# Performance work log

Hardware: AMD Instinct MI355X
Metric: run time of the kernel (lower is better)

The kernel has to match this reference:

```python
import jax, jax.numpy as jnp
import numpy as np

B, H, W, C = 4, 64, 64, 1280
NH = 16          # num heads
HD = C // NH     # 80 features per head
WS = 14          # window size
REL = 2 * WS - 1 # 27 relative-position entries per axis
EPS = 1e-6


def setup_inputs() -> dict:
    key = jax.random.key(0)
    ks = jax.random.split(key, 16)
    s = 0.02
    return {
        "imagelike_bhwc": jax.random.normal(ks[0], (B, H, W, C), jnp.float32),
        "ln1_g": jnp.ones((C,), jnp.float32),
        "ln1_b": jnp.zeros((C,), jnp.float32),
        "qkv_w": jax.random.normal(ks[1], (C, 3 * C), jnp.float32) * s,
        "qkv_b": jnp.zeros((3 * C,), jnp.float32),
        "proj_w": jax.random.normal(ks[2], (C, C), jnp.float32) * s,
        "proj_b": jnp.zeros((C,), jnp.float32),
        "rel_pos_h": jax.random.normal(ks[3], (REL, HD), jnp.float32) * s,
        "rel_pos_w": jax.random.normal(ks[4], (REL, HD), jnp.float32) * s,
        "ln2_g": jnp.ones((C,), jnp.float32),
        "ln2_b": jnp.zeros((C,), jnp.float32),
        "mlp_w1": jax.random.normal(ks[5], (C, 4 * C), jnp.float32) * s,
        "mlp_b1": jnp.zeros((4 * C,), jnp.float32),
        "mlp_w2": jax.random.normal(ks[6], (4 * C, C), jnp.float32) * s,
        "mlp_b2": jnp.zeros((C,), jnp.float32),
    }


def _layernorm(t, g, b):
    mu = jnp.mean(t, axis=-1, keepdims=True)
    var = jnp.var(t, axis=-1, keepdims=True)
    return (t - mu) * jax.lax.rsqrt(var + EPS) * g + b


def reference(imagelike_bhwc, ln1_g, ln1_b, qkv_w, qkv_b, proj_w, proj_b,
              rel_pos_h, rel_pos_w, ln2_g, ln2_b, mlp_w1, mlp_b1, mlp_w2, mlp_b2):
    x = imagelike_bhwc
    b, h, w, c = x.shape
    hd = c // NH
    scale = hd ** -0.5
    # --- image -> windows (pad to multiple of WS) ---
    hp, wp = (-h) % WS, (-w) % WS
    xp = jnp.pad(x, ((0, 0), (0, hp), (0, wp), (0, 0)))
    Hp, Wp = h + hp, w + wp
    ny, nx = Hp // WS, Wp // WS
    win = xp.reshape(b, ny, WS, nx, WS, c).transpose(0, 1, 3, 2, 4, 5)
    win = win.reshape(b * ny * nx, WS, WS, c)      # (Bw, S, S, C)
    Bw, N = win.shape[0], WS * WS
    # --- pre-attention layernorm + qkv ---
    t = _layernorm(win, ln1_g, ln1_b)
    qkv = t.reshape(Bw, N, c) @ qkv_w + qkv_b      # (Bw, N, 3C)
    qkv = qkv.reshape(Bw, N, 3, NH, hd).transpose(2, 0, 3, 1, 4)  # (3,Bw,NH,N,hd)
    q, k, v = qkv[0], qkv[1], qkv[2]
    # --- scores + decomposed relative position bias ---
    attn = jnp.einsum('bhqd,bhkd->bhqk', q * scale, k)            # (Bw,NH,N,N)
    idx = jnp.arange(WS)[:, None] - jnp.arange(WS)[None, :] + (WS - 1)
    Rh = rel_pos_h[idx]                                           # (WS,WS,hd)
    Rw = rel_pos_w[idx]                                           # (WS,WS,hd)
    qr = q.reshape(Bw, NH, WS, WS, hd)
    bias_h = jnp.einsum('bnyxd,ykd->bnyxk', qr, Rh)               # (Bw,NH,WS,WS,WS)
    bias_w = jnp.einsum('bnyxd,xkd->bnyxk', qr, Rw)
    bias = (bias_h[..., :, None] + bias_w[..., None, :]).reshape(Bw, NH, N, N)
    attn = jax.nn.softmax(attn + bias, axis=-1)
    out = jnp.einsum('bhqk,bhkd->bhqd', attn, v)                  # (Bw,NH,N,hd)
    out = out.transpose(0, 2, 1, 3).reshape(Bw, WS, WS, c)
    out = out @ proj_w + proj_b
    attn_out = out + win                                          # residual 1
    # --- MLP ---
    t2 = _layernorm(attn_out, ln2_g, ln2_b)
    mlp = jax.nn.gelu(t2 @ mlp_w1 + mlp_b1, approximate=False) @ mlp_w2 + mlp_b2
    out = mlp + attn_out                                          # residual 2
    # --- windows -> image (remove padding) ---
    img = out.reshape(b, ny, nx, WS, WS, c).transpose(0, 1, 3, 2, 4, 5)
    img = img.reshape(b, Hp, Wp, c)
    return img[:, :h, :w, :]
```

## Files before the change

kernel.cpp:

```cpp
#include <hip/hip_runtime.h>

typedef __attribute__((ext_vector_type(8))) short short8;
typedef __attribute__((ext_vector_type(4))) float f32x4;

#define GLBP(p) ((const __attribute__((address_space(1))) void*)(p))
#define LDSP(p) ((__attribute__((address_space(3))) void*)(p))

__device__ __forceinline__ float bf2f(unsigned short u) {
  return __uint_as_float(((unsigned int)u) << 16);
}
__device__ __forceinline__ unsigned short f2bf(float f) {
  unsigned int u = __float_as_uint(f);
  u += 0x7fff + ((u >> 16) & 1);
  return (unsigned short)(u >> 16);
}

__device__ __forceinline__ void tok2pix(int gt, int& b, int& py, int& px) {
  int w = gt / 196, t = gt - w * 196;
  b = w / 25;
  int wr = w - b * 25;
  int wy = wr / 5, wx = wr - wy * 5;
  int ty = t / 14;
  py = wy * 14 + ty;
  px = wx * 14 + (t - ty * 14);
}

__global__ void k_transpose(const float* __restrict__ W, unsigned short* __restrict__ Wt,
                            int K, int N) {
  __shared__ float tile[32][33];
  int tx = threadIdx.x, ty = threadIdx.y;
  int n0 = blockIdx.x * 32, k0 = blockIdx.y * 32;
#pragma unroll
  for (int i = 0; i < 4; ++i)
    tile[ty + 8 * i][tx] = W[(size_t)(k0 + ty + 8 * i) * N + n0 + tx];
  __syncthreads();
#pragma unroll
  for (int i = 0; i < 4; ++i)
    Wt[(size_t)(n0 + ty + 8 * i) * K + k0 + tx] = f2bf(tile[tx][ty + 8 * i]);
}

__global__ __launch_bounds__(256) void k_ln1(const float* __restrict__ x,
                                             const float* __restrict__ g,
                                             const float* __restrict__ be,
                                             unsigned short* __restrict__ A1,
                                             int w0, int ctok) {
  int m = blockIdx.x * 4 + (threadIdx.x >> 6);
  int lane = threadIdx.x & 63;
  int b, py, px;
  tok2pix(w0 * 196 + m, b, py, px);
  bool valid = (m < ctok) && (py < 64) && (px < 64);
  const float* row = x + ((size_t)((b * 64 + py) * 64 + px)) * 1280;
  float v[20];
#pragma unroll
  for (int i = 0; i < 20; ++i) v[i] = valid ? row[lane + 64 * i] : 0.f;
  float s = 0.f, ss = 0.f;
#pragma unroll
  for (int i = 0; i < 20; ++i) { s += v[i]; ss += v[i] * v[i]; }
#pragma unroll
  for (int o = 32; o > 0; o >>= 1) { s += __shfl_down(s, o); ss += __shfl_down(ss, o); }
  s = __shfl(s, 0);
  ss = __shfl(ss, 0);
  float mu = s * (1.f / 1280.f);
  float var = ss * (1.f / 1280.f) - mu * mu;
  float rinv = rsqrtf(var + 1e-6f);
  unsigned short* o1 = A1 + (size_t)m * 1280;
#pragma unroll
  for (int i = 0; i < 20; ++i) {
    int c = lane + 64 * i;
    o1[c] = f2bf((v[i] - mu) * rinv * g[c] + be[c]);
  }
}

__global__ __launch_bounds__(256) void k_ln2(const float* __restrict__ AT,
                                             const float* __restrict__ g,
                                             const float* __restrict__ be,
                                             unsigned short* __restrict__ A2,
                                             int w0, int ctok) {
  int m = blockIdx.x * 4 + (threadIdx.x >> 6);
  int lane = threadIdx.x & 63;
  int b, py, px;
  tok2pix(w0 * 196 + m, b, py, px);
  bool valid = (m < ctok) && (py < 64) && (px < 64);
  const float* row = AT + ((size_t)((b * 64 + py) * 64 + px)) * 1280;
  float v[20];
#pragma unroll
  for (int i = 0; i < 20; ++i) v[i] = valid ? row[lane + 64 * i] : 0.f;
  float s = 0.f, ss = 0.f;
#pragma unroll
  for (int i = 0; i < 20; ++i) { s += v[i]; ss += v[i] * v[i]; }
#pragma unroll
  for (int o = 32; o > 0; o >>= 1) { s += __shfl_down(s, o); ss += __shfl_down(ss, o); }
  s = __shfl(s, 0);
  ss = __shfl(ss, 0);
  float mu = s * (1.f / 1280.f);
  float var = ss * (1.f / 1280.f) - mu * mu;
  float rinv = rsqrtf(var + 1e-6f);
  unsigned short* o1 = A2 + (size_t)m * 1280;
#pragma unroll
  for (int i = 0; i < 20; ++i) {
    int c = lane + 64 * i;
    o1[c] = f2bf((v[i] - mu) * rinv * g[c] + be[c]);
  }
}

template <int EPI>
__device__ __forceinline__ void gemm_body(const unsigned short* __restrict__ A,
                                          const unsigned short* __restrict__ Bt,
                                          int K, int N, int gx,
                                          const float* __restrict__ bias,
                                          void* __restrict__ outp, int ctok) {
  __shared__ __align__(16) char smem[73728];
  int tid = threadIdx.x;
  int w = tid >> 6, lane = tid & 63;
  int nwg = gridDim.x, bid = blockIdx.x;
  int q = nwg >> 3, r = nwg & 7;
  int xcd = bid & 7, loc = bid >> 3;
  int wg = (xcd < r ? xcd * (q + 1) : r * (q + 1) + (xcd - r) * q) + loc;
  int bx = wg % gx, by = wg / gx;
  int mBase = by * 256, nBase = bx * 128;
  int wr = w >> 2, wc = w & 3;
  int la = lane & 15, lg = lane >> 4;

  int srow = tid >> 2;
  int schunk = (tid & 3) ^ ((srow >> 1) & 3);
  const char* pa0 = (const char*)A + (size_t)(mBase + srow) * K * 2 + (schunk << 4);
  const char* pa1 = (const char*)A + (size_t)(mBase + 128 + srow) * K * 2 + (schunk << 4);
  const char* pb0 = (const char*)Bt + (size_t)(nBase + srow) * K * 2 + (schunk << 4);
  int ldst = tid * 16;

  auto STAGE = [&](int slot, size_t ko) {
    int b = slot * 24576;
    __builtin_amdgcn_global_load_lds(GLBP(pa0 + ko), LDSP(smem + b + ldst), 16, 0, 0);
    __builtin_amdgcn_global_load_lds(GLBP(pa1 + ko), LDSP(smem + b + 8192 + ldst), 16, 0, 0);
    __builtin_amdgcn_global_load_lds(GLBP(pb0 + ko), LDSP(smem + b + 16384 + ldst), 16, 0, 0);
  };

  int offA[8], offB[2];
#pragma unroll
  for (int m = 0; m < 8; ++m) {
    int rr = wr * 128 + m * 16 + la;
    offA[m] = rr * 64 + ((lg ^ ((rr >> 1) & 3)) << 4);
  }
#pragma unroll
  for (int n = 0; n < 2; ++n) {
    int rr = wc * 32 + n * 16 + la;
    offB[n] = 16384 + rr * 64 + ((lg ^ ((rr >> 1) & 3)) << 4);
  }

  const f32x4 z4 = {0.f, 0.f, 0.f, 0.f};
  f32x4 acc[8][2];
#pragma unroll
  for (int m = 0; m < 8; ++m)
#pragma unroll
    for (int n = 0; n < 2; ++n) acc[m][n] = z4;

  int NT = K >> 5;
  STAGE(0, 0);
  STAGE(1, 64);
  int rs = 0;
  for (int t = 0; t < NT; ++t) {
    if (t + 1 < NT)
      asm volatile("s_waitcnt vmcnt(3)" ::: "memory");
    else
      asm volatile("s_waitcnt vmcnt(0)" ::: "memory");
    __builtin_amdgcn_s_barrier();
    __builtin_amdgcn_sched_barrier(0);
    if (t + 2 < NT) {
      int ws = rs + 2;
      if (ws >= 3) ws -= 3;
      STAGE(ws, (size_t)(t + 2) * 64);
    }
    const char* buf = (const char*)smem + rs * 24576;
    short8 af[4], bfr[2];
#pragma unroll
    for (int n = 0; n < 2; ++n) bfr[n] = *(const short8*)(buf + offB[n]);
#pragma unroll
    for (int m = 0; m < 4; ++m) af[m] = *(const short8*)(buf + offA[m]);
    __builtin_amdgcn_s_setprio(1);
#pragma unroll
    for (int m = 0; m < 4; ++m)
#pragma unroll
      for (int n = 0; n < 2; ++n)
        acc[m][n] = __builtin_amdgcn_mfma_f32_16x16x32_bf16(af[m], bfr[n], acc[m][n], 0, 0, 0);
    __builtin_amdgcn_s_setprio(0);
    __builtin_amdgcn_sched_barrier(0);
#pragma unroll
    for (int m = 0; m < 4; ++m) af[m] = *(const short8*)(buf + offA[m + 4]);
    __builtin_amdgcn_s_setprio(1);
#pragma unroll
    for (int m = 0; m < 4; ++m)
#pragma unroll
      for (int n = 0; n < 2; ++n)
        acc[m + 4][n] = __builtin_amdgcn_mfma_f32_16x16x32_bf16(af[m], bfr[n], acc[m + 4][n], 0, 0, 0);
    __builtin_amdgcn_s_setprio(0);
    rs = (rs == 2) ? 0 : rs + 1;
  }

#pragma unroll
  for (int m = 0; m < 8; ++m) {
#pragma unroll
    for (int n = 0; n < 2; ++n) {
      int col = nBase + wc * 32 + n * 16 + la;
      float bcol = bias[col];
#pragma unroll
      for (int j = 0; j < 4; ++j) {
        int row = mBase + wr * 128 + m * 16 + lg * 4 + j;
        float v = acc[m][n][j] + bcol;
        if (EPI == 0) {
          if (row < ctok) {
            int wloc = row / 196, tt = row - wloc * 196;
            int which = col / 1280, cr = col - which * 1280;
            int nh = cr / 80, d = cr - nh * 80;
            ((unsigned short*)outp)[((((size_t)wloc * 16 + nh) * 3 + which) * 196 + tt) * 80 + d] =
                f2bf(v);
          }
        } else {
          float gg = 0.5f * v * (1.f + erff(v * 0.70710678118654752f));
          ((unsigned short*)outp)[(size_t)row * N + col] = f2bf(gg);
        }
      }
    }
  }
}

template <int EPI>
__device__ __forceinline__ void gemm128_body(const unsigned short* __restrict__ A,
                                             const unsigned short* __restrict__ Bt,
                                             int K, int N, int gx,
                                             const float* __restrict__ bias,
                                             float* __restrict__ outp,
                                             const float* __restrict__ xres,
                                             int w0, int ctok) {
  __shared__ __align__(16) char smem[49152];
  int tid = threadIdx.x;
  int w = tid >> 6, lane = tid & 63;
  int nwg = gridDim.x, bid = blockIdx.x;
  int q = nwg >> 3, r = nwg & 7;
  int xcd = bid & 7, loc = bid >> 3;
  int wg = (xcd < r ? xcd * (q + 1) : r * (q + 1) + (xcd - r) * q) + loc;
  int bx = wg % gx, by = wg / gx;
  int mBase = by * 128, nBase = bx * 128;
  int wr = w >> 1, wc = w & 1;
  int la = lane & 15, lg = lane >> 4;

  int srow = tid >> 2;
  int schunk = (tid & 3) ^ ((srow >> 1) & 3);
  const char* pa[2];
  const char* pb[2];
#pragma unroll
  for (int i = 0; i < 2; ++i) {
    pa[i] = (const char*)A + (size_t)(mBase + srow + i * 64) * K * 2 + (schunk << 4);
    pb[i] = (const char*)Bt + (size_t)(nBase + srow + i * 64) * K * 2 + (schunk << 4);
  }
  int ldst = tid * 16;

  auto STAGE = [&](int slot, size_t ko) {
    int b = slot * 16384;
#pragma unroll
    for (int i = 0; i < 2; ++i)
      __builtin_amdgcn_global_load_lds(GLBP(pa[i] + ko), LDSP(smem + b + i * 4096 + ldst), 16, 0, 0);
#pragma unroll
    for (int i = 0; i < 2; ++i)
      __builtin_amdgcn_global_load_lds(GLBP(pb[i] + ko), LDSP(smem + b + 8192 + i * 4096 + ldst), 16, 0, 0);
  };

  int offA[4], offB[4];
#pragma unroll
  for (int m = 0; m < 4; ++m) {
    int rr = wr * 64 + m * 16 + la;
    offA[m] = rr * 64 + ((lg ^ ((rr >> 1) & 3)) << 4);
  }
#pragma unroll
  for (int n = 0; n < 4; ++n) {
    int rr = wc * 64 + n * 16 + la;
    offB[n] = 8192 + rr * 64 + ((lg ^ ((rr >> 1) & 3)) << 4);
  }

  const f32x4 z4 = {0.f, 0.f, 0.f, 0.f};
  f32x4 acc[4][4];
#pragma unroll
  for (int m = 0; m < 4; ++m)
#pragma unroll
    for (int n = 0; n < 4; ++n) acc[m][n] = z4;

  int NT = K >> 5;
  STAGE(0, 0);
  STAGE(1, 64);
  int rs = 0;
  for (int t = 0; t < NT; ++t) {
    if (t + 1 < NT)
      asm volatile("s_waitcnt vmcnt(4)" ::: "memory");
    else
      asm volatile("s_waitcnt vmcnt(0)" ::: "memory");
    __builtin_amdgcn_s_barrier();
    __builtin_amdgcn_sched_barrier(0);
    if (t + 2 < NT) {
      int ws = rs + 2;
      if (ws >= 3) ws -= 3;
      STAGE(ws, (size_t)(t + 2) * 64);
    }
    const char* buf = (const char*)smem + rs * 16384;
    short8 af[4], bfr[4];
#pragma unroll
    for (int n = 0; n < 4; ++n) bfr[n] = *(const short8*)(buf + offB[n]);
#pragma unroll
    for (int m = 0; m < 4; ++m) af[m] = *(const short8*)(buf + offA[m]);
    __builtin_amdgcn_s_setprio(1);
#pragma unroll
    for (int m = 0; m < 4; ++m)
#pragma unroll
      for (int n = 0; n < 4; ++n)
        acc[m][n] = __builtin_amdgcn_mfma_f32_16x16x32_bf16(af[m], bfr[n], acc[m][n], 0, 0, 0);
    __builtin_amdgcn_s_setprio(0);
    rs = (rs == 2) ? 0 : rs + 1;
  }

#pragma unroll
  for (int m = 0; m < 4; ++m) {
#pragma unroll
    for (int n = 0; n < 4; ++n) {
      int col = nBase + wc * 64 + n * 16 + la;
      float bcol = bias[col];
#pragma unroll
      for (int j = 0; j < 4; ++j) {
        int row = mBase + wr * 64 + m * 16 + lg * 4 + j;
        if (row < ctok) {
          int b, py, px;
          tok2pix(w0 * 196 + row, b, py, px);
          if (py < 64 && px < 64) {
            size_t pix = ((size_t)((b * 64 + py) * 64 + px)) * 1280 + col;
            float v = acc[m][n][j] + bcol;
            if (EPI == 1)
              outp[pix] = v + xres[pix];
            else
              outp[pix] = v + outp[pix];
          }
        }
      }
    }
  }
}

__global__ __launch_bounds__(512, 4) void k_gqkv(const unsigned short* A, const unsigned short* Bt,
                                                 int K, int N, int gx, const float* bias, void* o,
                                                 int ct) {
  gemm_body<0>(A, Bt, K, N, gx, bias, o, ct);
}
__global__ __launch_bounds__(512, 4) void k_gmlp1(const unsigned short* A, const unsigned short* Bt,
                                                  int K, int N, int gx, const float* bias, void* o,
                                                  int ct) {
  gemm_body<2>(A, Bt, K, N, gx, bias, o, ct);
}
__global__ __launch_bounds__(256, 3) void k_gproj(const unsigned short* A, const unsigned short* Bt,
                                                  int K, int N, int gx, const float* bias, float* o,
                                                  const float* xr, int w0, int ct) {
  gemm128_body<1>(A, Bt, K, N, gx, bias, o, xr, w0, ct);
}
__global__ __launch_bounds__(256, 3) void k_gmlp2(const unsigned short* A, const unsigned short* Bt,
                                                  int K, int N, int gx, const float* bias, float* o,
                                                  const float* xr, int w0, int ct) {
  gemm128_body<3>(A, Bt, K, N, gx, bias, o, xr, w0, ct);
}

__global__ __launch_bounds__(512, 1) void k_attn(const unsigned short* __restrict__ qkv,
                                                 const float* __restrict__ rph,
                                                 const float* __restrict__ rpw,
                                                 unsigned short* __restrict__ AO) {
  __shared__ unsigned short Ks[208 * 104];
  __shared__ unsigned short Vt[80 * 232];
  __shared__ unsigned short Ps[8][16 * 232];
  __shared__ unsigned short Bls[196 * 28];
  int wh = blockIdx.x;
  int w = wh >> 4, nh = wh & 15;
  int tid = threadIdx.x, wid = tid >> 6, lane = tid & 63;
  int la = lane & 15, lg = lane >> 4;
  const unsigned short* qb = qkv + (size_t)wh * 47040;
  const unsigned short* kb = qb + 15680;
  const unsigned short* vb = qb + 31360;
  const short8 z8 = {0, 0, 0, 0, 0, 0, 0, 0};

  for (int c = tid; c < 208 * 13; c += 512) {
    int t = c / 13, seg = c - t * 13;
    short8 kv = z8;
    if (t < 196 && seg < 10) kv = *(const short8*)(kb + (size_t)t * 80 + seg * 8);
    *(short8*)(Ks + t * 104 + seg * 8) = kv;
  }
  for (int c = tid; c < 1960; c += 512) {
    int t = c / 10, d8 = (c - t * 10) * 8;
    short8 vv = *(const short8*)(vb + (size_t)t * 80 + d8);
#pragma unroll
    for (int e = 0; e < 8; ++e) Vt[(d8 + e) * 232 + t] = (unsigned short)vv[e];
  }
  for (int i = tid; i < 80 * 36; i += 512) Vt[(i / 36) * 232 + 196 + (i % 36)] = 0;
  for (int id = tid; id < 196 * 28; id += 512) {
    int t = id / 28, c = id - t * 28;
    int y = t / 14, xx = t - y * 14;
    const float* R = (c < 14) ? (rph + (size_t)(y - c + 13) * 80)
                              : (rpw + (size_t)(xx - (c - 14) + 13) * 80);
    const unsigned short* qq = qb + (size_t)t * 80;
    float acc = 0.f;
#pragma unroll
    for (int d8 = 0; d8 < 10; ++d8) {
      short8 qv = *(const short8*)(qq + d8 * 8);
      const float4* Rv = (const float4*)(R + d8 * 8);
      float4 ra = Rv[0], rb = Rv[1];
      acc += bf2f((unsigned short)qv[0]) * ra.x + bf2f((unsigned short)qv[1]) * ra.y +
             bf2f((unsigned short)qv[2]) * ra.z + bf2f((unsigned short)qv[3]) * ra.w +
             bf2f((unsigned short)qv[4]) * rb.x + bf2f((unsigned short)qv[5]) * rb.y +
             bf2f((unsigned short)qv[6]) * rb.z + bf2f((unsigned short)qv[7]) * rb.w;
    }
    Bls[id] = f2bf(acc);
  }
  __syncthreads();

  int kyv[13], kxv[13];
#pragma unroll
  for (int ci = 0; ci < 13; ++ci) {
    int key = ci * 16 + la;
    kyv[ci] = key / 14;
    kxv[ci] = key - kyv[ci] * 14;
  }

  const float scale = 0.111803398874989485f;
  const f32x4 z4 = {0.f, 0.f, 0.f, 0.f};
  unsigned short* P = Ps[wid];

  auto process = [&](int rb) {
    short8 qa[3];
    int tq = rb * 16 + la;
    if (tq >= 196) tq = 0;
#pragma unroll
    for (int kk = 0; kk < 3; ++kk) {
      int d = kk * 32 + lg * 8;
      qa[kk] = (kk < 2 || lg < 2) ? *(const short8*)(qb + (size_t)tq * 80 + d) : z8;
    }
    f32x4 s[13];
#pragma unroll
    for (int i = 0; i < 13; ++i) s[i] = z4;
#pragma unroll
    for (int kk = 0; kk < 3; ++kk) {
#pragma unroll
      for (int ni = 0; ni < 13; ++ni) {
        short8 bb = *(const short8*)(Ks + (ni * 16 + la) * 104 + kk * 32 + lg * 8);
        s[ni] = __builtin_amdgcn_mfma_f32_16x16x32_bf16(qa[kk], bb, s[ni], 0, 0, 0);
      }
    }
#pragma unroll
    for (int j = 0; j < 4; ++j) {
      int rloc = lg * 4 + j;
      int t = rb * 16 + rloc;
      bool tval = t < 196;
      const unsigned short* Bp = Bls + (tval ? t : 0) * 28;
      float v[13];
      float mx = -3e30f;
#pragma unroll
      for (int ci = 0; ci < 13; ++ci) {
        int key = ci * 16 + la;
        float val = s[ci][j] * scale;
        if (key < 196 && tval) val += bf2f(Bp[kyv[ci]]) + bf2f(Bp[14 + kxv[ci]]);
        if (key >= 196 || !tval) val = -3e30f;
        v[ci] = val;
        mx = fmaxf(mx, val);
      }
#pragma unroll
      for (int o = 1; o < 16; o <<= 1) mx = fmaxf(mx, __shfl_xor(mx, o));
      float sum = 0.f;
#pragma unroll
      for (int ci = 0; ci < 13; ++ci) {
        float e = __expf(v[ci] - mx);
        v[ci] = e;
        sum += e;
      }
#pragma unroll
      for (int o = 1; o < 16; o <<= 1) sum += __shfl_xor(sum, o);
      float inv = 1.f / sum;
#pragma unroll
      for (int ci = 0; ci < 13; ++ci) P[rloc * 232 + ci * 16 + la] = f2bf(v[ci] * inv);
      P[rloc * 232 + 208 + la] = 0;
    }
    f32x4 o5[5];
#pragma unroll
    for (int i = 0; i < 5; ++i) o5[i] = z4;
#pragma unroll
    for (int kc = 0; kc < 7; ++kc) {
      short8 aa = *(const short8*)(P + la * 232 + kc * 32 + lg * 8);
#pragma unroll
      for (int ni = 0; ni < 5; ++ni) {
        short8 bb = *(const short8*)(Vt + (ni * 16 + la) * 232 + kc * 32 + lg * 8);
        o5[ni] = __builtin_amdgcn_mfma_f32_16x16x32_bf16(aa, bb, o5[ni], 0, 0, 0);
      }
    }
#pragma unroll
    for (int ni = 0; ni < 5; ++ni)
#pragma unroll
      for (int j = 0; j < 4; ++j) {
        int t = rb * 16 + lg * 4 + j;
        if (t < 196)
          AO[((size_t)w * 196 + t) * 1280 + nh * 80 + ni * 16 + la] = f2bf(o5[ni][j]);
      }
  };

  process(wid);
  if (wid < 5) process(wid + 8);
}

extern "C" void kernel_launch(void* const* d_in, const int* in_sizes, int n_in,
                              void* d_out, int out_size, void* d_ws, size_t ws_size,
                              hipStream_t stream) {
  const float* x = (const float*)d_in[0];
  const float* ln1g = (const float*)d_in[1];
  const float* ln1b = (const float*)d_in[2];
  const float* qkvw = (const float*)d_in[3];
  const float* qkvb = (const float*)d_in[4];
  const float* projw = (const float*)d_in[5];
  const float* projb = (const float*)d_in[6];
  const float* rph = (const float*)d_in[7];
  const float* rpw = (const float*)d_in[8];
  const float* ln2g = (const float*)d_in[9];
  const float* ln2b = (const float*)d_in[10];
  const float* w1 = (const float*)d_in[11];
  const float* b1 = (const float*)d_in[12];
  const float* w2 = (const float*)d_in[13];
  const float* b2 = (const float*)d_in[14];
  float* out = (float*)d_out;

  const size_t woff = (3840ull * 1280 + 1280ull * 1280 + 5120ull * 1280 + 1280ull * 5120) * 2;
  const int NWopts[12] = {25, 20, 18, 16, 14, 12, 10, 8, 5, 4, 2, 1};
  int NW = 0, Mb = 0;
  for (int i = 0; i < 12; ++i) {
    int nw = NWopts[i];
    int mb = ((nw * 196 + 255) / 256) * 256;
    size_t tot = woff + (size_t)mb * 12800;
    if (tot <= ws_size) { NW = nw; Mb = mb; break; }
  }
  if (!NW) return;

  char* p = (char*)d_ws;
  unsigned short* qkvwT = (unsigned short*)p; p += 3840ull * 1280 * 2;
  unsigned short* projwT = (unsigned short*)p; p += 1280ull * 1280 * 2;
  unsigned short* w1T = (unsigned short*)p; p += 5120ull * 1280 * 2;
  unsigned short* w2T = (unsigned short*)p; p += 1280ull * 5120 * 2;
  unsigned short* A1 = (unsigned short*)p; p += (size_t)Mb * 2560;
  unsigned short* QKV = (unsigned short*)p; p += (size_t)Mb * 7680;
  unsigned short* AO = (unsigned short*)p;
  unsigned short* Hb = QKV;
  unsigned short* A2 = A1;

  k_transpose<<<dim3(120, 40), dim3(32, 8), 0, stream>>>(qkvw, qkvwT, 1280, 3840);
  k_transpose<<<dim3(40, 40), dim3(32, 8), 0, stream>>>(projw, projwT, 1280, 1280);
  k_transpose<<<dim3(160, 40), dim3(32, 8), 0, stream>>>(w1, w1T, 1280, 5120);
  k_transpose<<<dim3(40, 160), dim3(32, 8), 0, stream>>>(w2, w2T, 5120, 1280);

  int gy256 = Mb / 256, gy128 = Mb / 128;
  int nchunks = (100 + NW - 1) / NW;
  for (int c = 0; c < nchunks; ++c) {
    int w0 = c * NW;
    int cw = (100 - w0 < NW) ? (100 - w0) : NW;
    int ctok = cw * 196;
    k_ln1<<<Mb / 4, 256, 0, stream>>>(x, ln1g, ln1b, A1, w0, ctok);
    k_gqkv<<<30 * gy256, 512, 0, stream>>>(A1, qkvwT, 1280, 3840, 30, qkvb, (void*)QKV, ctok);
    k_attn<<<cw * 16, 512, 0, stream>>>(QKV, rph, rpw, AO);
    k_gproj<<<10 * gy128, 256, 0, stream>>>(AO, projwT, 1280, 1280, 10, projb, out, x, w0, ctok);
    k_ln2<<<Mb / 4, 256, 0, stream>>>(out, ln2g, ln2b, A2, w0, ctok);
    k_gmlp1<<<40 * gy256, 512, 0, stream>>>(A2, w1T, 1280, 5120, 40, b1, (void*)Hb, ctok);
    k_gmlp2<<<10 * gy128, 256, 0, stream>>>(Hb, w2T, 5120, 1280, 10, b2, out, nullptr, w0, ctok);
  }
}
```

Baseline: 1.873 ms.

## Fold rel-pos bias into QK MFMA, store residual as bf16 token buffer

The attention kernel now pre-scales K and appends one-hot columns to the K tile, with the rel-pos bias values appended to Q. The bias add therefore happens inside the QK MFMA instead of in per-element scalar gathers, and the K LDS layout uses XOR swizzling. The attention residual is written as a bf16 token-major buffer that LN2 and the MLP2 epilogue read. This replaces strided fp32 image-layout round trips but adds bf16 rounding to the residual path. Launch bounds on the 256-tile GEMMs drop from 4 to 2 waves, and workspace sizing is adjusted for the new buffer.

New measurement: 1.817 ms. 1.03x faster.

```diff
diff --git a/kernel.cpp b/kernel.cpp
--- a/kernel.cpp
+++ b/kernel.cpp
@@ -71,20 +71,16 @@
   }
 }
 
-__global__ __launch_bounds__(256) void k_ln2(const float* __restrict__ AT,
+__global__ __launch_bounds__(256) void k_ln2(const unsigned short* __restrict__ AT,
                                              const float* __restrict__ g,
                                              const float* __restrict__ be,
-                                             unsigned short* __restrict__ A2,
-                                             int w0, int ctok) {
+                                             unsigned short* __restrict__ A2) {
   int m = blockIdx.x * 4 + (threadIdx.x >> 6);
   int lane = threadIdx.x & 63;
-  int b, py, px;
-  tok2pix(w0 * 196 + m, b, py, px);
-  bool valid = (m < ctok) && (py < 64) && (px < 64);
-  const float* row = AT + ((size_t)((b * 64 + py) * 64 + px)) * 1280;
+  const unsigned short* row = AT + (size_t)m * 1280;
   float v[20];
 #pragma unroll
-  for (int i = 0; i < 20; ++i) v[i] = valid ? row[lane + 64 * i] : 0.f;
+  for (int i = 0; i < 20; ++i) v[i] = bf2f(row[lane + 64 * i]);
   float s = 0.f, ss = 0.f;
 #pragma unroll
   for (int i = 0; i < 20; ++i) { s += v[i]; ss += v[i] * v[i]; }
@@ -223,13 +219,24 @@
   }
 }
 
+__global__ __launch_bounds__(512, 2) void k_gqkv(const unsigned short* A, const unsigned short* Bt,
+                                                 int K, int N, int gx, const float* bias, void* o,
+                                                 int ct) {
+  gemm_body<0>(A, Bt, K, N, gx, bias, o, ct);
+}
+__global__ __launch_bounds__(512, 2) void k_gmlp1(const unsigned short* A, const unsigned short* Bt,
+                                                  int K, int N, int gx, const float* bias, void* o,
+                                                  int ct) {
+  gemm_body<2>(A, Bt, K, N, gx, bias, o, ct);
+}
+
 template <int EPI>
 __device__ __forceinline__ void gemm128_body(const unsigned short* __restrict__ A,
                                              const unsigned short* __restrict__ Bt,
                                              int K, int N, int gx,
                                              const float* __restrict__ bias,
-                                             float* __restrict__ outp,
-                                             const float* __restrict__ xres,
+                                             void* __restrict__ outp,
+                                             const void* __restrict__ res,
                                              int w0, int ctok) {
   __shared__ __align__(16) char smem[49152];
   int tid = threadIdx.x;
@@ -327,13 +334,16 @@
         if (row < ctok) {
           int b, py, px;
           tok2pix(w0 * 196 + row, b, py, px);
-          if (py < 64 && px < 64) {
-            size_t pix = ((size_t)((b * 64 + py) * 64 + px)) * 1280 + col;
-            float v = acc[m][n][j] + bcol;
-            if (EPI == 1)
-              outp[pix] = v + xres[pix];
-            else
-              outp[pix] = v + outp[pix];
+          bool pv = (py < 64 && px < 64);
+          float v = acc[m][n][j] + bcol;
+          if (EPI == 1) {
+            float wv = pv ? ((const float*)res)[((size_t)((b * 64 + py) * 64 + px)) * 1280 + col]
+                          : 0.f;
+            ((unsigned short*)outp)[(size_t)row * 1280 + col] = f2bf(v + wv);
+          } else {
+            if (pv)
+              ((float*)outp)[((size_t)((b * 64 + py) * 64 + px)) * 1280 + col] =
+                  v + bf2f(((const unsigned short*)res)[(size_t)row * 1280 + col]);
           }
         }
       }
@@ -341,32 +351,22 @@
   }
 }
 
-__global__ __launch_bounds__(512, 4) void k_gqkv(const unsigned short* A, const unsigned short* Bt,
-                                                 int K, int N, int gx, const float* bias, void* o,
-                                                 int ct) {
-  gemm_body<0>(A, Bt, K, N, gx, bias, o, ct);
-}
-__global__ __launch_bounds__(512, 4) void k_gmlp1(const unsigned short* A, const unsigned short* Bt,
+__global__ __launch_bounds__(256, 3) void k_gproj(const unsigned short* A, const unsigned short* Bt,
                                                   int K, int N, int gx, const float* bias, void* o,
-                                                  int ct) {
-  gemm_body<2>(A, Bt, K, N, gx, bias, o, ct);
-}
-__global__ __launch_bounds__(256, 3) void k_gproj(const unsigned short* A, const unsigned short* Bt,
-                                                  int K, int N, int gx, const float* bias, float* o,
-                                                  const float* xr, int w0, int ct) {
-  gemm128_body<1>(A, Bt, K, N, gx, bias, o, xr, w0, ct);
+                                                  const void* res, int w0, int ct) {
+  gemm128_body<1>(A, Bt, K, N, gx, bias, o, res, w0, ct);
 }
 __global__ __launch_bounds__(256, 3) void k_gmlp2(const unsigned short* A, const unsigned short* Bt,
-                                                  int K, int N, int gx, const float* bias, float* o,
-                                                  const float* xr, int w0, int ct) {
-  gemm128_body<3>(A, Bt, K, N, gx, bias, o, xr, w0, ct);
+                                                  int K, int N, int gx, const float* bias, void* o,
+                                                  const void* res, int w0, int ct) {
+  gemm128_body<3>(A, Bt, K, N, gx, bias, o, res, w0, ct);
 }
 
 __global__ __launch_bounds__(512, 1) void k_attn(const unsigned short* __restrict__ qkv,
                                                  const float* __restrict__ rph,
                                                  const float* __restrict__ rpw,
                                                  unsigned short* __restrict__ AO) {
-  __shared__ unsigned short Ks[208 * 104];
+  __shared__ unsigned short Ks[208 * 128];
   __shared__ unsigned short Vt[80 * 232];
   __shared__ unsigned short Ps[8][16 * 232];
   __shared__ unsigned short Bls[196 * 28];
@@ -378,12 +378,27 @@
   const unsigned short* kb = qb + 15680;
   const unsigned short* vb = qb + 31360;
   const short8 z8 = {0, 0, 0, 0, 0, 0, 0, 0};
-
-  for (int c = tid; c < 208 * 13; c += 512) {
-    int t = c / 13, seg = c - t * 13;
+  const float scale = 0.111803398874989485f;
+
+  for (int c = tid; c < 208 * 16; c += 512) {
+    int t = c >> 4, seg = c & 15;
     short8 kv = z8;
-    if (t < 196 && seg < 10) kv = *(const short8*)(kb + (size_t)t * 80 + seg * 8);
-    *(short8*)(Ks + t * 104 + seg * 8) = kv;
+    if (t < 196) {
+      if (seg < 10) {
+        short8 raw = *(const short8*)(kb + (size_t)t * 80 + seg * 8);
+#pragma unroll
+        for (int e = 0; e < 8; ++e)
+          kv[e] = (short)f2bf(bf2f((unsigned short)raw[e]) * scale);
+      } else if (seg < 14) {
+        int ky = t / 14, kx = t - ky * 14;
+#pragma unroll
+        for (int e = 0; e < 8; ++e) {
+          int col = seg * 8 + e;
+          kv[e] = (col == 80 + ky || col == 94 + kx) ? (short)0x3F80 : (short)0;
+        }
+      }
+    }
+    *(short8*)((char*)Ks + t * 256 + ((seg * 16) ^ ((t & 7) << 4))) = kv;
   }
   for (int c = tid; c < 1960; c += 512) {
     int t = c / 10, d8 = (c - t * 10) * 8;
@@ -413,52 +428,61 @@
   }
   __syncthreads();
 
-  int kyv[13], kxv[13];
-#pragma unroll
-  for (int ci = 0; ci < 13; ++ci) {
-    int key = ci * 16 + la;
-    kyv[ci] = key / 14;
-    kxv[ci] = key - kyv[ci] * 14;
-  }
-
-  const float scale = 0.111803398874989485f;
   const f32x4 z4 = {0.f, 0.f, 0.f, 0.f};
   unsigned short* P = Ps[wid];
 
   auto process = [&](int rb) {
-    short8 qa[3];
-    int tq = rb * 16 + la;
-    if (tq >= 196) tq = 0;
-#pragma unroll
-    for (int kk = 0; kk < 3; ++kk) {
-      int d = kk * 32 + lg * 8;
-      qa[kk] = (kk < 2 || lg < 2) ? *(const short8*)(qb + (size_t)tq * 80 + d) : z8;
+    int t = rb * 16 + la;
+    bool tv = t < 196;
+    short8 qa[4];
+#pragma unroll
+    for (int kk = 0; kk < 2; ++kk)
+      qa[kk] = tv ? *(const short8*)(qb + (size_t)t * 80 + kk * 32 + lg * 8) : z8;
+    if (tv && lg < 2) {
+      qa[2] = *(const short8*)(qb + (size_t)t * 80 + 64 + lg * 8);
+    } else if (tv) {
+      short8 rr = z8;
+      int base = (lg - 2) * 8;
+#pragma unroll
+      for (int e = 0; e < 8; ++e) rr[e] = (short)Bls[t * 28 + base + e];
+      qa[2] = rr;
+    } else {
+      qa[2] = z8;
+    }
+    {
+      short8 rr = z8;
+      if (tv && lg == 0) {
+#pragma unroll
+        for (int e = 0; e < 8; ++e) rr[e] = (short)Bls[t * 28 + 16 + e];
+      } else if (tv && lg == 1) {
+#pragma unroll
+        for (int e = 0; e < 4; ++e) rr[e] = (short)Bls[t * 28 + 24 + e];
+      }
+      qa[3] = rr;
     }
     f32x4 s[13];
 #pragma unroll
     for (int i = 0; i < 13; ++i) s[i] = z4;
 #pragma unroll
-    for (int kk = 0; kk < 3; ++kk) {
+    for (int kk = 0; kk < 4; ++kk) {
+      int coff = (kk * 64 + lg * 16) ^ ((la & 7) << 4);
 #pragma unroll
       for (int ni = 0; ni < 13; ++ni) {
-        short8 bb = *(const short8*)(Ks + (ni * 16 + la) * 104 + kk * 32 + lg * 8);
+        short8 bb = *(const short8*)((char*)Ks + (ni * 16 + la) * 256 + coff);
         s[ni] = __builtin_amdgcn_mfma_f32_16x16x32_bf16(qa[kk], bb, s[ni], 0, 0, 0);
       }
     }
 #pragma unroll
     for (int j = 0; j < 4; ++j) {
       int rloc = lg * 4 + j;
-      int t = rb * 16 + rloc;
-      bool tval = t < 196;
-      const unsigned short* Bp = Bls + (tval ? t : 0) * 28;
+      int tt = rb * 16 + rloc;
+      bool ttv = tt < 196;
       float v[13];
       float mx = -3e30f;
 #pragma unroll
       for (int ci = 0; ci < 13; ++ci) {
         int key = ci * 16 + la;
-        float val = s[ci][j] * scale;
-        if (key < 196 && tval) val += bf2f(Bp[kyv[ci]]) + bf2f(Bp[14 + kxv[ci]]);
-        if (key >= 196 || !tval) val = -3e30f;
+        float val = (key < 196 && ttv) ? s[ci][j] : -3e30f;
         v[ci] = val;
         mx = fmaxf(mx, val);
       }
@@ -494,9 +518,9 @@
     for (int ni = 0; ni < 5; ++ni)
 #pragma unroll
       for (int j = 0; j < 4; ++j) {
-        int t = rb * 16 + lg * 4 + j;
-        if (t < 196)
-          AO[((size_t)w * 196 + t) * 1280 + nh * 80 + ni * 16 + la] = f2bf(o5[ni][j]);
+        int to = rb * 16 + lg * 4 + j;
+        if (to < 196)
+          AO[((size_t)w * 196 + to) * 1280 + nh * 80 + ni * 16 + la] = f2bf(o5[ni][j]);
       }
   };
 
@@ -525,12 +549,12 @@
   float* out = (float*)d_out;
 
   const size_t woff = (3840ull * 1280 + 1280ull * 1280 + 5120ull * 1280 + 1280ull * 5120) * 2;
-  const int NWopts[12] = {25, 20, 18, 16, 14, 12, 10, 8, 5, 4, 2, 1};
+  const int NWopts[11] = {25, 20, 16, 14, 12, 10, 8, 5, 4, 2, 1};
   int NW = 0, Mb = 0;
-  for (int i = 0; i < 12; ++i) {
+  for (int i = 0; i < 11; ++i) {
     int nw = NWopts[i];
     int mb = ((nw * 196 + 255) / 256) * 256;
-    size_t tot = woff + (size_t)mb * 12800;
+    size_t tot = woff + (size_t)mb * 15360;
     if (tot <= ws_size) { NW = nw; Mb = mb; break; }
   }
   if (!NW) return;
@@ -542,7 +566,8 @@
   unsigned short* w2T = (unsigned short*)p; p += 1280ull * 5120 * 2;
   unsigned short* A1 = (unsigned short*)p; p += (size_t)Mb * 2560;
   unsigned short* QKV = (unsigned short*)p; p += (size_t)Mb * 7680;
-  unsigned short* AO = (unsigned short*)p;
+  unsigned short* AO = (unsigned short*)p; p += (size_t)Mb * 2560;
+  unsigned short* ATTN = (unsigned short*)p;
   unsigned short* Hb = QKV;
   unsigned short* A2 = A1;
 
@@ -560,9 +585,11 @@
     k_ln1<<<Mb / 4, 256, 0, stream>>>(x, ln1g, ln1b, A1, w0, ctok);
     k_gqkv<<<30 * gy256, 512, 0, stream>>>(A1, qkvwT, 1280, 3840, 30, qkvb, (void*)QKV, ctok);
     k_attn<<<cw * 16, 512, 0, stream>>>(QKV, rph, rpw, AO);
-    k_gproj<<<10 * gy128, 256, 0, stream>>>(AO, projwT, 1280, 1280, 10, projb, out, x, w0, ctok);
-    k_ln2<<<Mb / 4, 256, 0, stream>>>(out, ln2g, ln2b, A2, w0, ctok);
+    k_gproj<<<10 * gy128, 256, 0, stream>>>(AO, projwT, 1280, 1280, 10, projb, (void*)ATTN,
+                                            (const void*)x, w0, ctok);
+    k_ln2<<<Mb / 4, 256, 0, stream>>>(ATTN, ln2g, ln2b, A2);
     k_gmlp1<<<40 * gy256, 512, 0, stream>>>(A2, w1T, 1280, 5120, 40, b1, (void*)Hb, ctok);
-    k_gmlp2<<<10 * gy128, 256, 0, stream>>>(Hb, w2T, 5120, 1280, 10, b2, out, nullptr, w0, ctok);
-  }
-}
+    k_gmlp2<<<10 * gy128, 256, 0, stream>>>(Hb, w2T, 5120, 1280, 10, b2, (void*)out,
+                                            (const void*)ATTN, w0, ctok);
+  }
+}
```
